# Kernel tuning notes

Measured on AMD Instinct MI355X. Metric: run time of the kernel, lower is better.

## Reference

```python
import jax, jax.numpy as jnp
import numpy as np

B = 32          # number of trees (batch)
N_LEAVES = 512  # complete binary tree -> 2*N_LEAVES-1 nodes per tree
IN_DIM = 1024
MEM = 1024


def setup_inputs() -> dict:
    key = jax.random.key(0)
    k1, k2, k3, k4 = jax.random.split(key, 4)
    s = 0.02
    inputs = jax.random.normal(k1, (B, N_LEAVES, IN_DIM), jnp.float32)
    w_fioux = jax.random.normal(k2, (4 * MEM, IN_DIM), jnp.float32) * s
    # rand_init: bias zero except first mem_dim entries set to 1 (forget-gate bias)
    b_fioux = jnp.zeros((4 * MEM,), jnp.float32).at[:MEM].set(1.0)
    w_iouh = jax.random.normal(k3, (3 * MEM, 2 * MEM), jnp.float32) * s
    w_fh = jax.random.normal(k4, (2 * MEM, 2 * MEM), jnp.float32) * s
    return {"inputs": inputs, "w_fioux": w_fioux, "b_fioux": b_fioux,
            "w_iouh": w_iouh, "w_fh": w_fh}


def _node_forward(x, child_c, child_h, w_fioux, b_fioux, w_iouh, w_fh):
    # x: [B, n, IN_DIM]; child_c/child_h: [B, n, 2*MEM] (left || right)
    fioux = x @ w_fioux.T + b_fioux                      # [B, n, 4M]
    fx, ix, ox, ux = jnp.split(fioux, 4, axis=-1)        # each [B, n, M]
    ih, oh, uh = jnp.split(child_h @ w_iouh.T, 3, axis=-1)
    i = jax.nn.sigmoid(ix + ih)
    o = jax.nn.sigmoid(ox + oh)
    u = jnp.tanh(ux + uh)
    # f gates: fx repeated for both children + fh(child_h)
    f = jax.nn.sigmoid(jnp.concatenate([fx, fx], axis=-1) + child_h @ w_fh.T)
    fc = f * child_c                                     # [B, n, 2M]
    c = i * u + fc[..., :MEM] + fc[..., MEM:]            # sum over the 2 children
    h = o * jnp.tanh(c)
    return c, h


def reference(inputs, w_fioux, b_fioux, w_iouh, w_fh):
    # Leaves: x = word input, child states are zeros
    z = jnp.zeros((B, N_LEAVES, 2 * MEM), inputs.dtype)
    c, h = _node_forward(inputs, z, z, w_fioux, b_fioux, w_iouh, w_fh)
    n = N_LEAVES
    # Internal nodes, level by level (log2(N_LEAVES) fixed iterations):
    # x = zeros (internal nodes have no token input), children are adjacent pairs.
    while n > 1:
        n //= 2
        child_c = c.reshape(B, n, 2 * MEM)   # [left_c || right_c]
        child_h = h.reshape(B, n, 2 * MEM)
        x = jnp.zeros((B, n, IN_DIM), inputs.dtype)
        c, h = _node_forward(x, child_c, child_h, w_fioux, b_fioux, w_iouh, w_fh)
    return h[:, 0, :]  # root hidden state, [B, MEM]
```

## Files before the change

### kernel.cpp

```cpp
#include <hip/hip_runtime.h>
#include <cstdint>
#include <cstddef>


typedef __attribute__((ext_vector_type(8))) short bf16x8;
typedef __attribute__((ext_vector_type(4))) float f32x4;

__device__ __forceinline__ float sig_(float x) { return 1.0f / (1.0f + __expf(-x)); }

__device__ __forceinline__ unsigned short f2bf_(float x) {
    union { float f; uint32_t u; } v; v.f = x;
    uint32_t r = v.u + 0x7fffu + ((v.u >> 16) & 1u);
    return (unsigned short)(r >> 16);
}
__device__ __forceinline__ float bf2f_(unsigned short u) {
    union { uint32_t u; float f; } v; v.u = ((uint32_t)u) << 16; return v.f;
}

#define GL16(g, l) __builtin_amdgcn_global_load_lds( \
    (const __attribute__((address_space(1))) void*)(g), \
    (__attribute__((address_space(3))) void*)(l), 16, 0, 0)

__global__ __launch_bounds__(512, 2)
void gemm320f(const unsigned short* __restrict__ A,
              const unsigned short* __restrict__ Wp,
              const float* __restrict__ b,
              const unsigned short* __restrict__ c_prev,
              unsigned short* __restrict__ c_out,
              unsigned short* __restrict__ h_out,
              int M)
{
    __shared__ unsigned short lA[4 * 8192];
    __shared__ unsigned short lB[4 * 10240];
    const int lda = 2048;

    const int orig = blockIdx.x + 16 * blockIdx.y;
    const int xcd  = orig & 7;
    const int pos  = orig >> 3;
    const int bx   = xcd * 2 + (pos & 1);
    const int by   = pos >> 1;

    const int tid = threadIdx.x;
    const int ln  = tid & 63;
    const int wv  = tid >> 6;
    const int wrp = wv >> 2;
    const int wcp = wv & 3;
    const int row0 = by * 256;
    const int colb = bx * 320;
    const bool five = (wv < 4);

    const int rowS = tid >> 2;
    const int gS   = (tid & 3) ^ ((tid >> 3) & 3);
    const unsigned short* a0 = A + (size_t)min(row0 + rowS,       M - 1) * lda + gS * 8;
    const unsigned short* a1 = A + (size_t)min(row0 + rowS + 128, M - 1) * lda + gS * 8;
    const unsigned short* w0 = Wp + (size_t)(colb + rowS)       * lda + gS * 8;
    const unsigned short* w1 = Wp + (size_t)(colb + rowS + 128) * lda + gS * 8;
    const unsigned short* w2 = Wp + (size_t)(colb + 256 + ((tid & 255) >> 2)) * lda + gS * 8;
    const int ld0 = tid * 8;
    const int ld1 = tid * 8 + 4096;
    const int ld2 = (tid & 255) * 8 + 8192;

    int offA[8], offB[5];
    #pragma unroll
    for (int i = 0; i < 8; ++i) {
        const int r = wrp * 128 + i * 16 + (ln & 15);
        offA[i] = r * 32 + ((ln >> 4) ^ ((r >> 1) & 3)) * 8;
    }
    #pragma unroll
    for (int g = 0; g < 5; ++g) {
        const int r = g * 64 + wcp * 16 + (ln & 15);
        offB[g] = r * 32 + ((ln >> 4) ^ ((r >> 1) & 3)) * 8;
    }

    f32x4 acc[8][5] = {};
    const int P = 64;

#define ISSUE_F(kh) do { \
    const int _sl = (kh) & 3; \
    const size_t _ko = (size_t)(kh) * 32; \
    GL16(a0 + _ko, lA + _sl * 8192 + ld0); \
    GL16(a1 + _ko, lA + _sl * 8192 + ld1); \
    GL16(w0 + _ko, lB + _sl * 10240 + ld0); \
    GL16(w1 + _ko, lB + _sl * 10240 + ld1); \
    if (five) GL16(w2 + _ko, lB + _sl * 10240 + ld2); \
} while (0)

    ISSUE_F(0); ISSUE_F(1); ISSUE_F(2);
    if (five) asm volatile("s_waitcnt vmcnt(10)" ::: "memory");
    else      asm volatile("s_waitcnt vmcnt(8)"  ::: "memory");
    asm volatile("s_barrier" ::: "memory");

    for (int p = 0; p < P; ++p) {
        const unsigned short* pa = lA + (p & 3) * 8192;
        const unsigned short* pb = lB + (p & 3) * 10240;
        bf16x8 bf[5], af[4], ag[4];
        #pragma unroll
        for (int g = 0; g < 5; ++g) bf[g] = *(const bf16x8*)(pb + offB[g]);
        #pragma unroll
        for (int i = 0; i < 4; ++i) af[i] = *(const bf16x8*)(pa + offA[i]);
        #pragma unroll
        for (int i = 0; i < 4; ++i) ag[i] = *(const bf16x8*)(pa + offA[4 + i]);
        if (p <= P - 4) ISSUE_F(p + 3);
        __builtin_amdgcn_s_setprio(1);
        #pragma unroll
        for (int m = 0; m < 4; ++m)
            #pragma unroll
            for (int g = 0; g < 5; ++g)
                acc[m][g] = __builtin_amdgcn_mfma_f32_16x16x32_bf16(af[m], bf[g], acc[m][g], 0, 0, 0);
        #pragma unroll
        for (int m = 0; m < 4; ++m)
            #pragma unroll
            for (int g = 0; g < 5; ++g)
                acc[4 + m][g] = __builtin_amdgcn_mfma_f32_16x16x32_bf16(ag[m], bf[g], acc[4 + m][g], 0, 0, 0);
        __builtin_amdgcn_s_setprio(0);
        if (p <= P - 4) {
            if (five) asm volatile("s_waitcnt vmcnt(10)" ::: "memory");
            else      asm volatile("s_waitcnt vmcnt(8)"  ::: "memory");
        } else if (p == P - 3) {
            if (five) asm volatile("s_waitcnt vmcnt(5)" ::: "memory");
            else      asm volatile("s_waitcnt vmcnt(4)" ::: "memory");
        } else if (p == P - 2) {
            asm volatile("s_waitcnt vmcnt(0)" ::: "memory");
        }
        if (p < P - 1) asm volatile("s_barrier" ::: "memory");
    }
#undef ISSUE_F

    const int jg = bx * 64 + wcp * 16 + (ln & 15);
    const float bi = b[1024 + jg];
    const float bo = b[2048 + jg];
    const float bu = b[3072 + jg];
    const float bff = b[jg];
    #pragma unroll
    for (int mi = 0; mi < 8; ++mi) {
        #pragma unroll
        for (int rg = 0; rg < 4; ++rg) {
            const int r = row0 + wrp * 128 + mi * 16 + (ln >> 4) * 4 + rg;
            if (r < M) {
                const float cl = bf2f_(c_prev[(size_t)r * 2048 + jg]);
                const float cr = bf2f_(c_prev[(size_t)r * 2048 + 1024 + jg]);
                const float iv = sig_(acc[mi][0][rg] + bi);
                const float ov = sig_(acc[mi][1][rg] + bo);
                const float uv = tanhf(acc[mi][2][rg] + bu);
                const float flv = sig_(acc[mi][3][rg] + bff);
                const float frv = sig_(acc[mi][4][rg] + bff);
                const float c = iv * uv + flv * cl + frv * cr;
                const float h = ov * tanhf(c);
                c_out[(size_t)r * 1024 + jg] = f2bf_(c);
                h_out[(size_t)r * 1024 + jg] = f2bf_(h);
            }
        }
    }
}

__global__ __launch_bounds__(256, 2)
void gemm_leaff(const unsigned short* __restrict__ A,
                const unsigned short* __restrict__ Wp,
                const float* __restrict__ b,
                unsigned short* __restrict__ c_out,
                unsigned short* __restrict__ h_out)
{
    __shared__ unsigned short lA[3 * 4096];
    __shared__ unsigned short lB[3 * 6144];
    const int lda = 1024;

    const int orig = blockIdx.x + 16 * blockIdx.y;
    const int xcd  = orig & 7;
    const int pos  = orig >> 3;
    const int bx   = xcd * 2 + (pos & 1);
    const int by   = pos >> 1;

    if ((pos >> 5) & 1) asm volatile("s_sleep 10" ::: "memory");

    const int tid = threadIdx.x;
    const int ln  = tid & 63;
    const int wv  = tid >> 6;
    const int wrp = wv >> 1;
    const int wcp = wv & 1;
    const int row0 = by * 128;
    const int colb = bx * 192;

    const int rowS = tid >> 2;
    const int gS   = (tid & 3) ^ ((tid >> 3) & 3);
    const unsigned short* a0 = A + (size_t)(row0 + rowS) * lda + gS * 8;
    const unsigned short* a1 = a0 + (size_t)64 * lda;
    const unsigned short* w0 = Wp + (size_t)(colb + rowS) * lda + gS * 8;
    const unsigned short* w1 = w0 + (size_t)64 * lda;
    const unsigned short* w2 = w0 + (size_t)128 * lda;
    const int ld0 = tid * 8;

    int offA[4], offB[6];
    #pragma unroll
    for (int i = 0; i < 4; ++i) {
        const int r = wrp * 64 + i * 16 + (ln & 15);
        offA[i] = r * 32 + ((ln >> 4) ^ ((r >> 1) & 3)) * 8;
    }
    #pragma unroll
    for (int grp = 0; grp < 2; ++grp)
        #pragma unroll
        for (int g = 0; g < 3; ++g) {
            const int r = wcp * 96 + grp * 48 + g * 16 + (ln & 15);
            offB[grp * 3 + g] = r * 32 + ((ln >> 4) ^ ((r >> 1) & 3)) * 8;
        }

    f32x4 acc[4][6] = {};
    const int P = 32;

#define ISSUE_L(sl, kh) do { \
    const size_t _ko = (size_t)(kh) * 32; \
    GL16(a0 + _ko, lA + (sl) * 4096 + ld0); \
    GL16(a1 + _ko, lA + (sl) * 4096 + 2048 + ld0); \
    GL16(w0 + _ko, lB + (sl) * 6144 + ld0); \
    GL16(w1 + _ko, lB + (sl) * 6144 + 2048 + ld0); \
    GL16(w2 + _ko, lB + (sl) * 6144 + 4096 + ld0); \
} while (0)

    ISSUE_L(0, 0); ISSUE_L(1, 1);
    asm volatile("s_waitcnt vmcnt(5)" ::: "memory");
    asm volatile("s_barrier" ::: "memory");

    int rd = 0, is = 2;
    for (int p = 0; p < P; ++p) {
        const unsigned short* pa = lA + rd * 4096;
        const unsigned short* pb = lB + rd * 6144;
        bf16x8 bf[6], af[4];
        #pragma unroll
        for (int g = 0; g < 6; ++g) bf[g] = *(const bf16x8*)(pb + offB[g]);
        #pragma unroll
        for (int i = 0; i < 4; ++i) af[i] = *(const bf16x8*)(pa + offA[i]);
        if (p <= P - 3) ISSUE_L(is, p + 2);
        __builtin_amdgcn_s_setprio(1);
        #pragma unroll
        for (int m = 0; m < 4; ++m)
            #pragma unroll
            for (int g = 0; g < 6; ++g)
                acc[m][g] = __builtin_amdgcn_mfma_f32_16x16x32_bf16(af[m], bf[g], acc[m][g], 0, 0, 0);
        __builtin_amdgcn_s_setprio(0);
        if (p <= P - 3)      asm volatile("s_waitcnt vmcnt(5)" ::: "memory");
        else if (p == P - 2) asm volatile("s_waitcnt vmcnt(0)" ::: "memory");
        if (p < P - 1) asm volatile("s_barrier" ::: "memory");
        rd = (rd == 2) ? 0 : rd + 1;
        is = (is == 2) ? 0 : is + 1;
    }
#undef ISSUE_L

    #pragma unroll
    for (int grp = 0; grp < 2; ++grp) {
        const int j = bx * 64 + wcp * 32 + grp * 16 + (ln & 15);
        const float bi = b[1024 + j];
        const float bo = b[2048 + j];
        const float bu = b[3072 + j];
        #pragma unroll
        for (int mi = 0; mi < 4; ++mi) {
            #pragma unroll
            for (int rg = 0; rg < 4; ++rg) {
                const int r = row0 + wrp * 64 + mi * 16 + (ln >> 4) * 4 + rg;
                const float cv = sig_(acc[mi][grp * 3 + 0][rg] + bi) * tanhf(acc[mi][grp * 3 + 2][rg] + bu);
                const float hv = sig_(acc[mi][grp * 3 + 1][rg] + bo) * tanhf(cv);
                c_out[(size_t)r * 1024 + j] = f2bf_(cv);
                h_out[(size_t)r * 1024 + j] = f2bf_(hv);
            }
        }
    }
}

__global__ __launch_bounds__(512, 2)
void gemm256(const unsigned short* __restrict__ A,
             const unsigned short* __restrict__ W,
             unsigned short* __restrict__ C, int M, int N, int lda, int Klen)
{
    __shared__ unsigned short lA[4 * 8192];
    __shared__ unsigned short lB[4 * 8192];

    const int gx = gridDim.x, gy = gridDim.y;
    int id = blockIdx.x + gx * (blockIdx.y + gy * blockIdx.z);
    {
        const int nwg = gx * gy * gridDim.z;
        const int q = nwg >> 3, r = nwg & 7, x = id & 7, i = id >> 3;
        id = (x < r ? x * (q + 1) : r * (q + 1) + (x - r) * q) + i;
    }
    const int bz  = id / (gx * gy);
    const int rem = id - bz * gx * gy;
    const int by  = rem / gx;
    const int bx  = rem - by * gx;

    const int tid = threadIdx.x;
    const int ln  = tid & 63;
    const int wv  = tid >> 6;
    const int wrp = wv >> 2;
    const int wcp = wv & 3;
    const int row0 = by * 256;
    const int colb = bx * 256;
    const int kbase = bz * Klen;
    C += (size_t)bz * M * N;

    const int rowS = tid >> 2;
    const int gS   = (tid & 3) ^ ((tid >> 3) & 3);
    const unsigned short* a0 = A + (size_t)min(row0 + rowS,       M - 1) * lda + kbase + gS * 8;
    const unsigned short* a1 = A + (size_t)min(row0 + rowS + 128, M - 1) * lda + kbase + gS * 8;
    const unsigned short* b0 = W + (size_t)(colb + rowS)       * lda + kbase + gS * 8;
    const unsigned short* b1 = W + (size_t)(colb + rowS + 128) * lda + kbase + gS * 8;
    const int ld0 = tid * 8;
    const int ld1 = tid * 8 + 4096;

    int offA[8], offB[4];
    #pragma unroll
    for (int i = 0; i < 8; ++i) {
        const int r = wrp * 128 + i * 16 + (ln & 15);
        offA[i] = r * 32 + ((ln >> 4) ^ ((r >> 1) & 3)) * 8;
    }
    #pragma unroll
    for (int i = 0; i < 4; ++i) {
        const int r = wcp * 64 + i * 16 + (ln & 15);
        offB[i] = r * 32 + ((ln >> 4) ^ ((r >> 1) & 3)) * 8;
    }

    f32x4 acc[8][4] = {};
    const int P = Klen >> 5;

#define ISSUE_KH(kh) do { \
    const int _sl = (kh) & 3; \
    const size_t _ko = (size_t)(kh) * 32; \
    GL16(a0 + _ko, lA + _sl * 8192 + ld0); \
    GL16(a1 + _ko, lA + _sl * 8192 + ld1); \
    GL16(b0 + _ko, lB + _sl * 8192 + ld0); \
    GL16(b1 + _ko, lB + _sl * 8192 + ld1); \
} while (0)

    ISSUE_KH(0); ISSUE_KH(1); ISSUE_KH(2);
    asm volatile("s_waitcnt vmcnt(8)" ::: "memory");
    asm volatile("s_barrier" ::: "memory");

    for (int p = 0; p < P; ++p) {
        const unsigned short* pa = lA + (p & 3) * 8192;
        const unsigned short* pb = lB + (p & 3) * 8192;
        bf16x8 bf[4], af[4], ag[4];
        #pragma unroll
        for (int i = 0; i < 4; ++i) bf[i] = *(const bf16x8*)(pb + offB[i]);
        #pragma unroll
        for (int i = 0; i < 4; ++i) af[i] = *(const bf16x8*)(pa + offA[i]);
        #pragma unroll
        for (int i = 0; i < 4; ++i) ag[i] = *(const bf16x8*)(pa + offA[4 + i]);
        if (p <= P - 4) ISSUE_KH(p + 3);
        __builtin_amdgcn_s_setprio(1);
        #pragma unroll
        for (int m = 0; m < 4; ++m)
            #pragma unroll
            for (int n = 0; n < 4; ++n)
                acc[m][n] = __builtin_amdgcn_mfma_f32_16x16x32_bf16(af[m], bf[n], acc[m][n], 0, 0, 0);
        #pragma unroll
        for (int m = 0; m < 4; ++m)
            #pragma unroll
            for (int n = 0; n < 4; ++n)
                acc[4 + m][n] = __builtin_amdgcn_mfma_f32_16x16x32_bf16(ag[m], bf[n], acc[4 + m][n], 0, 0, 0);
        __builtin_amdgcn_s_setprio(0);
        if (p <= P - 4)      asm volatile("s_waitcnt vmcnt(8)" ::: "memory");
        else if (p == P - 3) asm volatile("s_waitcnt vmcnt(4)" ::: "memory");
        else if (p == P - 2) asm volatile("s_waitcnt vmcnt(0)" ::: "memory");
        if (p < P - 1) asm volatile("s_barrier" ::: "memory");
    }
#undef ISSUE_KH

    #pragma unroll
    for (int mi = 0; mi < 8; ++mi) {
        #pragma unroll
        for (int ni = 0; ni < 4; ++ni) {
            const int col = colb + wcp * 64 + ni * 16 + (ln & 15);
            #pragma unroll
            for (int rg = 0; rg < 4; ++rg) {
                const int r = row0 + wrp * 128 + mi * 16 + (ln >> 4) * 4 + rg;
                if (r < M) C[(size_t)r * N + col] = f2bf_(acc[mi][ni][rg]);
            }
        }
    }
}

__global__ void f2bf_vec(const float* __restrict__ src, unsigned short* __restrict__ dst, int n4)
{
    const int i = blockIdx.x * blockDim.x + threadIdx.x;
    if (i >= n4) return;
    const float4 v = ((const float4*)src)[i];
    ushort4 o;
    o.x = f2bf_(v.x); o.y = f2bf_(v.y); o.z = f2bf_(v.z); o.w = f2bf_(v.w);
    ((ushort4*)dst)[i] = o;
}

__global__ void build_wfxp(const float* __restrict__ w_fioux,
                           unsigned short* __restrict__ dst, int total4)
{
    const int idx = blockIdx.x * blockDim.x + threadIdx.x;
    if (idx >= total4) return;
    const int rp = idx >> 8;
    const int c4 = (idx & 255) << 2;
    const int t  = rp / 48;
    const int q  = rp - t * 48;
    const int g  = q >> 4;
    const int jj = q & 15;
    const float* src = w_fioux + (size_t)((g + 1) * 1024 + t * 16 + jj) * 1024;
    const float4 v = *(const float4*)(src + c4);
    ushort4 o;
    o.x = f2bf_(v.x); o.y = f2bf_(v.y); o.z = f2bf_(v.z); o.w = f2bf_(v.w);
    *(ushort4*)(dst + (size_t)rp * 1024 + c4) = o;
}

__global__ void build_wcatp(const float* __restrict__ w_iouh, const float* __restrict__ w_fh,
                            unsigned short* __restrict__ dst, int total4)
{
    const int idx = blockIdx.x * blockDim.x + threadIdx.x;
    if (idx >= total4) return;
    const int rp = idx >> 9;
    const int c4 = (idx & 511) << 2;
    const int t  = rp / 320;
    const int q  = rp - t * 320;
    const int g  = q >> 6;
    const int jj = q & 63;
    const int srow = t * 64 + jj;
    const float* src = (g < 3) ? (w_iouh + (size_t)(g * 1024 + srow) * 2048)
                               : (w_fh   + (size_t)((g - 3) * 1024 + srow) * 2048);
    const float4 v = *(const float4*)(src + c4);
    ushort4 o;
    o.x = f2bf_(v.x); o.y = f2bf_(v.y); o.z = f2bf_(v.z); o.w = f2bf_(v.w);
    *(ushort4*)(dst + (size_t)rp * 2048 + c4) = o;
}

__device__ __forceinline__ void acc4_(float* v, ushort4 u) {
    v[0] += bf2f_(u.x); v[1] += bf2f_(u.y); v[2] += bf2f_(u.z); v[3] += bf2f_(u.w);
}

__global__ void node_gates(const unsigned short* __restrict__ g, int S, size_t sstride,
                           const float* __restrict__ b,
                           const unsigned short* __restrict__ c_prev,
                           unsigned short* __restrict__ c_out,
                           unsigned short* __restrict__ h_bf,
                           float* __restrict__ h_f32, int rows)
{
    const int idx = blockIdx.x * blockDim.x + threadIdx.x;
    if (idx >= rows * 256) return;
    const int r = idx >> 8, q = (idx & 255) << 2;
    const int t = q >> 6, jj = q & 63;
    float vi[4] = {}, vo[4] = {}, vu[4] = {}, vfl[4] = {}, vfr[4] = {};
    const unsigned short* gr = g + (size_t)r * 5120 + t * 320 + jj;
    for (int s = 0; s < S; ++s, gr += sstride) {
        acc4_(vi,  *(const ushort4*)(gr));
        acc4_(vo,  *(const ushort4*)(gr + 64));
        acc4_(vu,  *(const ushort4*)(gr + 128));
        acc4_(vfl, *(const ushort4*)(gr + 192));
        acc4_(vfr, *(const ushort4*)(gr + 256));
    }
    const float* bi = b + 1024 + q;
    const float* bo = b + 2048 + q;
    const float* bu = b + 3072 + q;
    const float* bff = b + q;
    const ushort4 clu = *(const ushort4*)(c_prev + (size_t)r * 2048 + q);
    const ushort4 cru = *(const ushort4*)(c_prev + (size_t)r * 2048 + 1024 + q);
    const float cl[4] = { bf2f_(clu.x), bf2f_(clu.y), bf2f_(clu.z), bf2f_(clu.w) };
    const float cr[4] = { bf2f_(cru.x), bf2f_(cru.y), bf2f_(cru.z), bf2f_(cru.w) };

    ushort4 co, ho;
    float cv[4], hv[4];
    #pragma unroll
    for (int e = 0; e < 4; ++e) {
        const float c = sig_(vi[e] + bi[e]) * tanhf(vu[e] + bu[e])
                      + sig_(vfl[e] + bff[e]) * cl[e]
                      + sig_(vfr[e] + bff[e]) * cr[e];
        cv[e] = c;
        hv[e] = sig_(vo[e] + bo[e]) * tanhf(c);
    }
    co.x = f2bf_(cv[0]); co.y = f2bf_(cv[1]); co.z = f2bf_(cv[2]); co.w = f2bf_(cv[3]);
    ho.x = f2bf_(hv[0]); ho.y = f2bf_(hv[1]); ho.z = f2bf_(hv[2]); ho.w = f2bf_(hv[3]);
    *(ushort4*)(c_out + (size_t)r * 1024 + q) = co;
    *(ushort4*)(h_bf + (size_t)r * 1024 + q) = ho;
    if (h_f32) {
        float4 hf; hf.x = hv[0]; hf.y = hv[1]; hf.z = hv[2]; hf.w = hv[3];
        *(float4*)(h_f32 + (size_t)r * 1024 + q) = hf;
    }
}

extern "C" void kernel_launch(void* const* d_in, const int* in_sizes, int n_in,
                              void* d_out, int out_size, void* d_ws, size_t ws_size,
                              hipStream_t stream)
{
    const float* inputs  = (const float*)d_in[0];
    const float* w_fioux = (const float*)d_in[1];
    const float* b_fioux = (const float*)d_in[2];
    const float* w_iouh  = (const float*)d_in[3];
    const float* w_fh    = (const float*)d_in[4];
    float* out = (float*)d_out;

    unsigned short* us    = (unsigned short*)d_ws;
    unsigned short* c_a   = us;
    unsigned short* c_b   = c_a + (size_t)16777216;
    unsigned short* h_a   = c_b + (size_t)8388608;
    unsigned short* h_b   = h_a + (size_t)16777216;
    unsigned short* wfxP  = h_b + (size_t)8388608;
    unsigned short* wcatP = wfxP + (size_t)3145728;
    unsigned short* gbuf  = wcatP + (size_t)10485760;
    unsigned short* x_bf  = gbuf;

    f2bf_vec<<<16384, 256, 0, stream>>>(inputs, x_bf, 4194304);
    build_wfxp<<<3072, 256, 0, stream>>>(w_fioux, wfxP, 786432);
    build_wcatp<<<10240, 256, 0, stream>>>(w_iouh, w_fh, wcatP, 5120 * 512);

    gemm_leaff<<<dim3(16, 128), 256, 0, stream>>>(x_bf, wfxP, b_fioux, c_a, h_a);

    unsigned short *hp = h_a, *cp = c_a, *hn = h_b, *cn = c_b;
    for (int n = 256; n >= 64; n >>= 1) {
        const int m = 32 * n;
        gemm320f<<<dim3(16, m / 256), 512, 0, stream>>>(hp, wcatP, b_fioux, cp, cn, hn, m);
        unsigned short* t;
        t = hp; hp = hn; hn = t;
        t = cp; cp = cn; cn = t;
    }

    for (int n = 32; n >= 1; n >>= 1) {
        const int m = 32 * n;
        const int S = (m >= 512) ? 4 : 8;
        const int Klen = 2048 / S;
        gemm256<<<dim3(20, (m + 255) / 256, S), 512, 0, stream>>>(
            hp, wcatP, gbuf, m, 5120, 2048, Klen);
        node_gates<<<m, 256, 0, stream>>>(
            gbuf, S, (size_t)m * 5120, b_fioux, cp, cn, hn,
            (n == 1) ? out : nullptr, m);
        unsigned short* t;
        t = hp; hp = hn; hn = t;
        t = cp; cp = cn; cn = t;
    }
    (void)in_sizes; (void)n_in; (void)out_size; (void)ws_size;
}
```

Before: 682.6 us.

## Double-buffer LDS fragments in registers to overlap MFMA with LDS reads

For the non-five (four-group) GEMM path, the main loop is software-pipelined with two register sets of A/B fragments. Each step issues the MFMAs for the previously loaded set while reading the next set from LDS. Each step then waits on lgkmcnt(0) before the barrier. The aim is to hide LDS read latency behind matrix-core work, at the cost of twice the fragment registers. That extra register use may raise pressure at two blocks per CU. The five-group path keeps the original loop, restated through helper macros.

Result: slower. 720.2 us (+5.5%).

```diff
diff --git a/kernel.cpp b/kernel.cpp
--- a/kernel.cpp
+++ b/kernel.cpp
@@ -85,46 +85,84 @@
     if (five) GL16(w2 + _ko, lB + _sl * 10240 + ld2); \
 } while (0)
 
+#define LADDER_E(p) do { \
+    if ((p) <= P - 4)      asm volatile("s_waitcnt vmcnt(10)" ::: "memory"); \
+    else if ((p) == P - 3) asm volatile("s_waitcnt vmcnt(5)"  ::: "memory"); \
+    else if ((p) == P - 2) asm volatile("s_waitcnt vmcnt(0)"  ::: "memory"); \
+} while (0)
+
+#define LADDER_L(p) do { \
+    if ((p) <= P - 4)      asm volatile("s_waitcnt vmcnt(8)" ::: "memory"); \
+    else if ((p) == P - 3) asm volatile("s_waitcnt vmcnt(4)" ::: "memory"); \
+    else if ((p) == P - 2) asm volatile("s_waitcnt vmcnt(0)" ::: "memory"); \
+} while (0)
+
+#define READ_SET(BF, AF, AG, pa, pb) do { \
+    _Pragma("unroll") for (int _g = 0; _g < 5; ++_g) BF[_g] = *(const bf16x8*)((pb) + offB[_g]); \
+    _Pragma("unroll") for (int _i = 0; _i < 4; ++_i) AF[_i] = *(const bf16x8*)((pa) + offA[_i]); \
+    _Pragma("unroll") for (int _i = 0; _i < 4; ++_i) AG[_i] = *(const bf16x8*)((pa) + offA[4 + _i]); \
+} while (0)
+
+#define MFMA_SET(BF, AF, AG) do { \
+    __builtin_amdgcn_s_setprio(1); \
+    _Pragma("unroll") for (int _m = 0; _m < 4; ++_m) \
+        _Pragma("unroll") for (int _g = 0; _g < 5; ++_g) \
+            acc[_m][_g] = __builtin_amdgcn_mfma_f32_16x16x32_bf16(AF[_m], BF[_g], acc[_m][_g], 0, 0, 0); \
+    _Pragma("unroll") for (int _m = 0; _m < 4; ++_m) \
+        _Pragma("unroll") for (int _g = 0; _g < 5; ++_g) \
+            acc[4 + _m][_g] = __builtin_amdgcn_mfma_f32_16x16x32_bf16(AG[_m], BF[_g], acc[4 + _m][_g], 0, 0, 0); \
+    __builtin_amdgcn_s_setprio(0); \
+} while (0)
+
     ISSUE_F(0); ISSUE_F(1); ISSUE_F(2);
     if (five) asm volatile("s_waitcnt vmcnt(10)" ::: "memory");
     else      asm volatile("s_waitcnt vmcnt(8)"  ::: "memory");
     asm volatile("s_barrier" ::: "memory");
 
-    for (int p = 0; p < P; ++p) {
-        const unsigned short* pa = lA + (p & 3) * 8192;
-        const unsigned short* pb = lB + (p & 3) * 10240;
-        bf16x8 bf[5], af[4], ag[4];
-        #pragma unroll
-        for (int g = 0; g < 5; ++g) bf[g] = *(const bf16x8*)(pb + offB[g]);
-        #pragma unroll
-        for (int i = 0; i < 4; ++i) af[i] = *(const bf16x8*)(pa + offA[i]);
-        #pragma unroll
-        for (int i = 0; i < 4; ++i) ag[i] = *(const bf16x8*)(pa + offA[4 + i]);
-        if (p <= P - 4) ISSUE_F(p + 3);
-        __builtin_amdgcn_s_setprio(1);
-        #pragma unroll
-        for (int m = 0; m < 4; ++m)
-            #pragma unroll
-            for (int g = 0; g < 5; ++g)
-                acc[m][g] = __builtin_amdgcn_mfma_f32_16x16x32_bf16(af[m], bf[g], acc[m][g], 0, 0, 0);
-        #pragma unroll
-        for (int m = 0; m < 4; ++m)
-            #pragma unroll
-            for (int g = 0; g < 5; ++g)
-                acc[4 + m][g] = __builtin_amdgcn_mfma_f32_16x16x32_bf16(ag[m], bf[g], acc[4 + m][g], 0, 0, 0);
-        __builtin_amdgcn_s_setprio(0);
-        if (p <= P - 4) {
-            if (five) asm volatile("s_waitcnt vmcnt(10)" ::: "memory");
-            else      asm volatile("s_waitcnt vmcnt(8)"  ::: "memory");
-        } else if (p == P - 3) {
-            if (five) asm volatile("s_waitcnt vmcnt(5)" ::: "memory");
-            else      asm volatile("s_waitcnt vmcnt(4)" ::: "memory");
-        } else if (p == P - 2) {
-            asm volatile("s_waitcnt vmcnt(0)" ::: "memory");
+    if (five) {
+        for (int p = 0; p < P; ++p) {
+            const unsigned short* pa = lA + (p & 3) * 8192;
+            const unsigned short* pb = lB + (p & 3) * 10240;
+            bf16x8 bf[5], af[4], ag[4];
+            READ_SET(bf, af, ag, pa, pb);
+            if (p <= P - 4) ISSUE_F(p + 3);
+            MFMA_SET(bf, af, ag);
+            LADDER_E(p);
+            if (p < P - 1) asm volatile("s_barrier" ::: "memory");
         }
-        if (p < P - 1) asm volatile("s_barrier" ::: "memory");
+    } else {
+        bf16x8 bfA[5], afA[4], agA[4], bfB[5], afB[4], agB[4];
+        for (int t = 0; t < P / 2; ++t) {
+            {
+                const int p = 2 * t;
+                if (p > 0) MFMA_SET(bfB, afB, agB);
+                if (p <= P - 4) ISSUE_F(p + 3);
+                const unsigned short* pa = lA + (p & 3) * 8192;
+                const unsigned short* pb = lB + (p & 3) * 10240;
+                READ_SET(bfA, afA, agA, pa, pb);
+                asm volatile("s_waitcnt lgkmcnt(0)" ::: "memory");
+                LADDER_L(p);
+                if (p < P - 1) asm volatile("s_barrier" ::: "memory");
+            }
+            {
+                const int p = 2 * t + 1;
+                MFMA_SET(bfA, afA, agA);
+                if (p <= P - 4) ISSUE_F(p + 3);
+                const unsigned short* pa = lA + (p & 3) * 8192;
+                const unsigned short* pb = lB + (p & 3) * 10240;
+                READ_SET(bfB, afB, agB, pa, pb);
+                asm volatile("s_waitcnt lgkmcnt(0)" ::: "memory");
+                LADDER_L(p);
+                if (p < P - 1) asm volatile("s_barrier" ::: "memory");
+            }
+        }
+        MFMA_SET(bfB, afB, agB);
     }
 #undef ISSUE_F
+#undef LADDER_E
+#undef LADDER_L
+#undef READ_SET
+#undef MFMA_SET
 
     const int jg = bx * 64 + wcp * 16 + (ln & 15);
     const float bi = b[1024 + jg];
```

## Add 512-row fused gate GEMM for first internal level and reassign later levels

Applied to the files above, without the earlier changes.

Adds a 1024-thread kernel with 512-row tiles and a 3-stage LDS ring, used for the largest internal level (M=8192) so each block reuses its weight tile across twice as many rows and fewer blocks reread the weights. The 256-row fused kernel now handles only the M=4096 level. The n=64 level moves to the split-K gemm256 path with S=2 plus a separate gate kernel. The trade-off is one block per CU with a shallower prefetch, and an extra gbuf round trip at n=64.

New measurement: 2.520 ms. 269% more time.

```diff
diff --git a/kernel.cpp b/kernel.cpp
--- a/kernel.cpp
+++ b/kernel.cpp
@@ -21,17 +21,17 @@
     (const __attribute__((address_space(1))) void*)(g), \
     (__attribute__((address_space(3))) void*)(l), 16, 0, 0)
 
-__global__ __launch_bounds__(512, 2)
-void gemm320f(const unsigned short* __restrict__ A,
-              const unsigned short* __restrict__ Wp,
-              const float* __restrict__ b,
-              const unsigned short* __restrict__ c_prev,
-              unsigned short* __restrict__ c_out,
-              unsigned short* __restrict__ h_out,
-              int M)
-{
-    __shared__ unsigned short lA[4 * 8192];
-    __shared__ unsigned short lB[4 * 10240];
+__global__ __launch_bounds__(1024, 1)
+void gemm512(const unsigned short* __restrict__ A,
+             const unsigned short* __restrict__ Wp,
+             const float* __restrict__ b,
+             const unsigned short* __restrict__ c_prev,
+             unsigned short* __restrict__ c_out,
+             unsigned short* __restrict__ h_out,
+             int M)
+{
+    __shared__ unsigned short lA[3 * 16384];
+    __shared__ unsigned short lB[3 * 10240];
     const int lda = 2048;
 
     const int orig = blockIdx.x + 16 * blockIdx.y;
@@ -45,20 +45,17 @@
     const int wv  = tid >> 6;
     const int wrp = wv >> 2;
     const int wcp = wv & 3;
-    const int row0 = by * 256;
+    const int row0 = by * 512;
     const int colb = bx * 320;
-    const bool five = (wv < 4);
+    const bool four = (wv < 4);
 
     const int rowS = tid >> 2;
     const int gS   = (tid & 3) ^ ((tid >> 3) & 3);
-    const unsigned short* a0 = A + (size_t)min(row0 + rowS,       M - 1) * lda + gS * 8;
-    const unsigned short* a1 = A + (size_t)min(row0 + rowS + 128, M - 1) * lda + gS * 8;
-    const unsigned short* w0 = Wp + (size_t)(colb + rowS)       * lda + gS * 8;
-    const unsigned short* w1 = Wp + (size_t)(colb + rowS + 128) * lda + gS * 8;
-    const unsigned short* w2 = Wp + (size_t)(colb + 256 + ((tid & 255) >> 2)) * lda + gS * 8;
+    const unsigned short* a0 = A + (size_t)(row0 + rowS) * lda + gS * 8;
+    const unsigned short* a1 = a0 + (size_t)256 * lda;
+    const unsigned short* b0 = Wp + (size_t)(colb + rowS) * lda + gS * 8;
+    const unsigned short* b1 = Wp + (size_t)min(colb + 256 + rowS, 5119) * lda + gS * 8;
     const int ld0 = tid * 8;
-    const int ld1 = tid * 8 + 4096;
-    const int ld2 = (tid & 255) * 8 + 8192;
 
     int offA[8], offB[5];
     #pragma unroll
@@ -75,24 +72,23 @@
     f32x4 acc[8][5] = {};
     const int P = 64;
 
-#define ISSUE_F(kh) do { \
-    const int _sl = (kh) & 3; \
+#define ISSUE_5(sl, kh) do { \
     const size_t _ko = (size_t)(kh) * 32; \
-    GL16(a0 + _ko, lA + _sl * 8192 + ld0); \
-    GL16(a1 + _ko, lA + _sl * 8192 + ld1); \
-    GL16(w0 + _ko, lB + _sl * 10240 + ld0); \
-    GL16(w1 + _ko, lB + _sl * 10240 + ld1); \
-    if (five) GL16(w2 + _ko, lB + _sl * 10240 + ld2); \
+    GL16(a0 + _ko, lA + (sl) * 16384 + ld0); \
+    GL16(a1 + _ko, lA + (sl) * 16384 + 8192 + ld0); \
+    GL16(b0 + _ko, lB + (sl) * 10240 + ld0); \
+    if (four) GL16(b1 + _ko, lB + (sl) * 10240 + 8192 + ld0); \
 } while (0)
 
-    ISSUE_F(0); ISSUE_F(1); ISSUE_F(2);
-    if (five) asm volatile("s_waitcnt vmcnt(10)" ::: "memory");
-    else      asm volatile("s_waitcnt vmcnt(8)"  ::: "memory");
+    ISSUE_5(0, 0); ISSUE_5(1, 1);
+    if (four) asm volatile("s_waitcnt vmcnt(4)" ::: "memory");
+    else      asm volatile("s_waitcnt vmcnt(3)" ::: "memory");
     asm volatile("s_barrier" ::: "memory");
 
+    int rd = 0, is = 2;
     for (int p = 0; p < P; ++p) {
-        const unsigned short* pa = lA + (p & 3) * 8192;
-        const unsigned short* pb = lB + (p & 3) * 10240;
+        const unsigned short* pa = lA + rd * 16384;
+        const unsigned short* pb = lB + rd * 10240;
         bf16x8 bf[5], af[4], ag[4];
         #pragma unroll
         for (int g = 0; g < 5; ++g) bf[g] = *(const bf16x8*)(pb + offB[g]);
@@ -100,7 +96,7 @@
         for (int i = 0; i < 4; ++i) af[i] = *(const bf16x8*)(pa + offA[i]);
         #pragma unroll
         for (int i = 0; i < 4; ++i) ag[i] = *(const bf16x8*)(pa + offA[4 + i]);
-        if (p <= P - 4) ISSUE_F(p + 3);
+        if (p <= P - 3) ISSUE_5(is, p + 2);
         __builtin_amdgcn_s_setprio(1);
         #pragma unroll
         for (int m = 0; m < 4; ++m)
@@ -113,18 +109,17 @@
             for (int g = 0; g < 5; ++g)
                 acc[4 + m][g] = __builtin_amdgcn_mfma_f32_16x16x32_bf16(ag[m], bf[g], acc[4 + m][g], 0, 0, 0);
         __builtin_amdgcn_s_setprio(0);
-        if (p <= P - 4) {
-            if (five) asm volatile("s_waitcnt vmcnt(10)" ::: "memory");
-            else      asm volatile("s_waitcnt vmcnt(8)"  ::: "memory");
-        } else if (p == P - 3) {
-            if (five) asm volatile("s_waitcnt vmcnt(5)" ::: "memory");
-            else      asm volatile("s_waitcnt vmcnt(4)" ::: "memory");
+        if (p <= P - 3) {
+            if (four) asm volatile("s_waitcnt vmcnt(4)" ::: "memory");
+            else      asm volatile("s_waitcnt vmcnt(3)" ::: "memory");
         } else if (p == P - 2) {
             asm volatile("s_waitcnt vmcnt(0)" ::: "memory");
         }
         if (p < P - 1) asm volatile("s_barrier" ::: "memory");
-    }
-#undef ISSUE_F
+        rd = (rd == 2) ? 0 : rd + 1;
+        is = (is == 2) ? 0 : is + 1;
+    }
+#undef ISSUE_5
 
     const int jg = bx * 64 + wcp * 16 + (ln & 15);
     const float bi = b[1024 + jg];
@@ -153,6 +148,138 @@
     }
 }
 
+__global__ __launch_bounds__(512, 2)
+void gemm320f(const unsigned short* __restrict__ A,
+              const unsigned short* __restrict__ Wp,
+              const float* __restrict__ b,
+              const unsigned short* __restrict__ c_prev,
+              unsigned short* __restrict__ c_out,
+              unsigned short* __restrict__ h_out,
+              int M)
+{
+    __shared__ unsigned short lA[4 * 8192];
+    __shared__ unsigned short lB[4 * 10240];
+    const int lda = 2048;
+
+    const int orig = blockIdx.x + 16 * blockIdx.y;
+    const int xcd  = orig & 7;
+    const int pos  = orig >> 3;
+    const int bx   = xcd * 2 + (pos & 1);
+    const int by   = pos >> 1;
+
+    const int tid = threadIdx.x;
+    const int ln  = tid & 63;
+    const int wv  = tid >> 6;
+    const int wrp = wv >> 2;
+    const int wcp = wv & 3;
+    const int row0 = by * 256;
+    const int colb = bx * 320;
+    const bool five = (wv < 4);
+
+    const int rowS = tid >> 2;
+    const int gS   = (tid & 3) ^ ((tid >> 3) & 3);
+    const unsigned short* a0 = A + (size_t)min(row0 + rowS,       M - 1) * lda + gS * 8;
+    const unsigned short* a1 = A + (size_t)min(row0 + rowS + 128, M - 1) * lda + gS * 8;
+    const unsigned short* w0 = Wp + (size_t)(colb + rowS)       * lda + gS * 8;
+    const unsigned short* w1 = Wp + (size_t)(colb + rowS + 128) * lda + gS * 8;
+    const unsigned short* w2 = Wp + (size_t)(colb + 256 + ((tid & 255) >> 2)) * lda + gS * 8;
+    const int ld0 = tid * 8;
+    const int ld1 = tid * 8 + 4096;
+    const int ld2 = (tid & 255) * 8 + 8192;
+
+    int offA[8], offB[5];
+    #pragma unroll
+    for (int i = 0; i < 8; ++i) {
+        const int r = wrp * 128 + i * 16 + (ln & 15);
+        offA[i] = r * 32 + ((ln >> 4) ^ ((r >> 1) & 3)) * 8;
+    }
+    #pragma unroll
+    for (int g = 0; g < 5; ++g) {
+        const int r = g * 64 + wcp * 16 + (ln & 15);
+        offB[g] = r * 32 + ((ln >> 4) ^ ((r >> 1) & 3)) * 8;
+    }
+
+    f32x4 acc[8][5] = {};
+    const int P = 64;
+
+#define ISSUE_F(kh) do { \
+    const int _sl = (kh) & 3; \
+    const size_t _ko = (size_t)(kh) * 32; \
+    GL16(a0 + _ko, lA + _sl * 8192 + ld0); \
+    GL16(a1 + _ko, lA + _sl * 8192 + ld1); \
+    GL16(w0 + _ko, lB + _sl * 10240 + ld0); \
+    GL16(w1 + _ko, lB + _sl * 10240 + ld1); \
+    if (five) GL16(w2 + _ko, lB + _sl * 10240 + ld2); \
+} while (0)
+
+    ISSUE_F(0); ISSUE_F(1); ISSUE_F(2);
+    if (five) asm volatile("s_waitcnt vmcnt(10)" ::: "memory");
+    else      asm volatile("s_waitcnt vmcnt(8)"  ::: "memory");
+    asm volatile("s_barrier" ::: "memory");
+
+    for (int p = 0; p < P; ++p) {
+        const unsigned short* pa = lA + (p & 3) * 8192;
+        const unsigned short* pb = lB + (p & 3) * 10240;
+        bf16x8 bf[5], af[4], ag[4];
+        #pragma unroll
+        for (int g = 0; g < 5; ++g) bf[g] = *(const bf16x8*)(pb + offB[g]);
+        #pragma unroll
+        for (int i = 0; i < 4; ++i) af[i] = *(const bf16x8*)(pa + offA[i]);
+        #pragma unroll
+        for (int i = 0; i < 4; ++i) ag[i] = *(const bf16x8*)(pa + offA[4 + i]);
+        if (p <= P - 4) ISSUE_F(p + 3);
+        __builtin_amdgcn_s_setprio(1);
+        #pragma unroll
+        for (int m = 0; m < 4; ++m)
+            #pragma unroll
+            for (int g = 0; g < 5; ++g)
+                acc[m][g] = __builtin_amdgcn_mfma_f32_16x16x32_bf16(af[m], bf[g], acc[m][g], 0, 0, 0);
+        #pragma unroll
+        for (int m = 0; m < 4; ++m)
+            #pragma unroll
+            for (int g = 0; g < 5; ++g)
+                acc[4 + m][g] = __builtin_amdgcn_mfma_f32_16x16x32_bf16(ag[m], bf[g], acc[4 + m][g], 0, 0, 0);
+        __builtin_amdgcn_s_setprio(0);
+        if (p <= P - 4) {
+            if (five) asm volatile("s_waitcnt vmcnt(10)" ::: "memory");
+            else      asm volatile("s_waitcnt vmcnt(8)"  ::: "memory");
+        } else if (p == P - 3) {
+            if (five) asm volatile("s_waitcnt vmcnt(5)" ::: "memory");
+            else      asm volatile("s_waitcnt vmcnt(4)" ::: "memory");
+        } else if (p == P - 2) {
+            asm volatile("s_waitcnt vmcnt(0)" ::: "memory");
+        }
+        if (p < P - 1) asm volatile("s_barrier" ::: "memory");
+    }
+#undef ISSUE_F
+
+    const int jg = bx * 64 + wcp * 16 + (ln & 15);
+    const float bi = b[1024 + jg];
+    const float bo = b[2048 + jg];
+    const float bu = b[3072 + jg];
+    const float bff = b[jg];
+    #pragma unroll
+    for (int mi = 0; mi < 8; ++mi) {
+        #pragma unroll
+        for (int rg = 0; rg < 4; ++rg) {
+            const int r = row0 + wrp * 128 + mi * 16 + (ln >> 4) * 4 + rg;
+            if (r < M) {
+                const float cl = bf2f_(c_prev[(size_t)r * 2048 + jg]);
+                const float cr = bf2f_(c_prev[(size_t)r * 2048 + 1024 + jg]);
+                const float iv = sig_(acc[mi][0][rg] + bi);
+                const float ov = sig_(acc[mi][1][rg] + bo);
+                const float uv = tanhf(acc[mi][2][rg] + bu);
+                const float flv = sig_(acc[mi][3][rg] + bff);
+                const float frv = sig_(acc[mi][4][rg] + bff);
+                const float c = iv * uv + flv * cl + frv * cr;
+                const float h = ov * tanhf(c);
+                c_out[(size_t)r * 1024 + jg] = f2bf_(c);
+                h_out[(size_t)r * 1024 + jg] = f2bf_(h);
+            }
+        }
+    }
+}
+
 __global__ __launch_bounds__(256, 2)
 void gemm_leaff(const unsigned short* __restrict__ A,
                 const unsigned short* __restrict__ Wp,
@@ -504,17 +631,17 @@
     gemm_leaff<<<dim3(16, 128), 256, 0, stream>>>(x_bf, wfxP, b_fioux, c_a, h_a);
 
     unsigned short *hp = h_a, *cp = c_a, *hn = h_b, *cn = c_b;
-    for (int n = 256; n >= 64; n >>= 1) {
+    gemm512<<<dim3(16, 16), 1024, 0, stream>>>(hp, wcatP, b_fioux, cp, cn, hn, 8192);
+    { unsigned short* t = hp; hp = hn; hn = t; t = cp; cp = cn; cn = t; }
+    gemm320f<<<dim3(16, 16), 512, 0, stream>>>(hp, wcatP, b_fioux, cp, cn, hn, 4096);
+    { unsigned short* t = hp; hp = hn; hn = t; t = cp; cp = cn; cn = t; }
+
+    for (int n = 64; n >= 1; n >>= 1) {
         const int m = 32 * n;
-        gemm320f<<<dim3(16, m / 256), 512, 0, stream>>>(hp, wcatP, b_fioux, cp, cn, hn, m);
-        unsigned short* t;
-        t = hp; hp = hn; hn = t;
-        t = cp; cp = cn; cn = t;
-    }
-
-    for (int n = 32; n >= 1; n >>= 1) {
-        const int m = 32 * n;
-        const int S = (m >= 512) ? 4 : 8;
+        int S;
+        if (m >= 2048)      S = 2;
+        else if (m >= 512)  S = 4;
+        else                S = 8;
         const int Klen = 2048 / S;
         gemm256<<<dim3(20, (m + 255) / 256, S), 512, 0, stream>>>(
             hp, wcatP, gbuf, m, 5120, 2048, Klen);
```
